# Optimization experiments

Measured on AMD Instinct MI355X. Metric: run time of the kernel, lower is better.

The kernel has to match this reference:

```python
import jax, jax.numpy as jnp
import numpy as np

N = 100000   # nodes
E = 1600000  # edges
IN = 32      # input_dim == num_concepts
H = 128      # h_dim == num_concepts * dim_per_concept
C = 32       # num_concepts
D = 4        # dim_per_concept
G = 32       # g_dim of per-concept MLPs
LAMBDAV = 1e-3


def _spmm(edge_src, edge_dst, edge_val, x):
    # sparse adjacency matmul: out[d] = sum_{edges e: dst(e)=d} val(e) * x[src(e)]
    return jax.ops.segment_sum(edge_val[:, None] * x[edge_src], edge_dst, num_segments=N)


def setup_inputs() -> dict:
    key = jax.random.key(0)
    ks = jax.random.split(key, 20)
    s = lambda shape: 1.0 / np.sqrt(shape[-1] if len(shape) > 1 else 1)
    inp = {
        'X': jax.random.normal(ks[0], (N, IN), jnp.float32),
        'label': jax.random.uniform(ks[1], (N, C), jnp.float32),
        'edge_val': jax.random.uniform(ks[2], (E,), jnp.float32),
        'noise': jax.random.normal(ks[3], (N, C, D), jnp.float32),
        'W_base': jax.random.normal(ks[4], (IN, H), jnp.float32) / np.sqrt(IN),
        'W_mean': jax.random.normal(ks[5], (H, H), jnp.float32) / np.sqrt(H),
        'W_logstd': jax.random.normal(ks[6], (H, H), jnp.float32) / np.sqrt(H),
        'A': 0.05 * jax.random.normal(ks[7], (C, C), jnp.float32),  # keep I - A^T well-conditioned
        'Wz1': jax.random.normal(ks[8], (C, D, G), jnp.float32) / np.sqrt(D),
        'bz1': jax.random.normal(ks[9], (C, G), jnp.float32) * 0.01,
        'Wz2': jax.random.normal(ks[10], (C, G, D), jnp.float32) / np.sqrt(G),
        'bz2': jax.random.normal(ks[11], (C, D), jnp.float32) * 0.01,
        'Wl1': jax.random.normal(ks[12], (C, 1, G), jnp.float32),
        'bl1': jax.random.normal(ks[13], (C, G), jnp.float32) * 0.01,
        'Wl2': jax.random.normal(ks[14], (C, G, 1), jnp.float32) / np.sqrt(G),
        'bl2': jax.random.normal(ks[15], (C, 1), jnp.float32) * 0.01,
        'Wrec': jax.random.normal(ks[16], (H, IN), jnp.float32) / np.sqrt(H),
        'brec': jax.random.normal(ks[17], (IN,), jnp.float32) * 0.01,
        'edge_src': jax.random.randint(ks[18], (E,), 0, N),
        'edge_dst': jax.random.randint(ks[19], (E,), 0, N),
    }
    return inp


def reference(X, label, edge_val, noise, W_base, W_mean, W_logstd, A,
              Wz1, bz1, Wz2, bz2, Wl1, bl1, Wl2, bl2, Wrec, brec,
              edge_src, edge_dst):
    # ---- sparse GCN encoder (x branch): GraphConvSparse = act(spmm(adj, x @ W)) ----
    hidden = jax.nn.relu(_spmm(edge_src, edge_dst, edge_val, X @ W_base))   # [N, H]
    e_m = _spmm(edge_src, edge_dst, edge_val, hidden @ W_mean)              # [N, H]
    _ = _spmm(edge_src, edge_dst, edge_val, hidden @ W_logstd)              # computed then discarded (e_v := ones) in source
    e_m = e_m.reshape(N, C, D)                                              # [N, C, D]

    # ---- CausalDAG: z = (I - A^T)^{-1} epsilon along the concept axis ----
    I = jnp.eye(C, dtype=X.dtype)
    Cmat = jnp.linalg.inv(I - A.T)                                          # [C, C]
    z_m = jnp.einsum('ck,nkd->ncd', Cmat, e_m)                              # [N, C, D]

    # mask: A^T @ x along concept axis
    masked_z_m = jnp.einsum('ck,nkd->ncd', A.T, z_m)                        # [N, C, D]
    masked_label = jnp.einsum('ck,nk->nc', A.T, label)[..., None]           # [N, C, 1]

    # g_z: per-concept MLP Linear(D,G)-ELU-Linear(G,D), weights stacked over concepts
    hz = jax.nn.elu(jnp.einsum('ncd,cdg->ncg', masked_z_m, Wz1) + bz1[None])
    masked_z_m = jnp.einsum('ncg,cgd->ncd', hz, Wz2) + bz2[None]            # [N, C, D]

    # g_label: per-concept MLP Linear(1,G)-ELU-Linear(G,1)
    hl = jax.nn.elu(jnp.einsum('nce,ceg->ncg', masked_label, Wl1) + bl1[None])
    pred_label = (jnp.einsum('ncg,cge->nce', hl, Wl2) + bl2[None])[..., 0]  # [N, C]

    # conditional_sample_gaussian with v = e_v * lambdav, e_v = ones
    z = masked_z_m + jnp.sqrt(jnp.asarray(LAMBDAV, X.dtype)) * noise        # [N, C, D]

    # pred_x / reconst_X head
    rec_x = z.reshape(N, H) @ Wrec + brec                                   # [N, IN]
    return rec_x, pred_label
```

## Files before the change

### kernel.cpp

```cpp
#include <hip/hip_runtime.h>
#include <hip/hip_bf16.h>

#define N_NODES 100000
#define N_EDGES 1600000
#define NBUCK   391

static __device__ __forceinline__ float us2f(unsigned short u) {
    union { unsigned int i; float f; } cv; cv.i = ((unsigned int)u) << 16; return cv.f;
}
static __device__ __forceinline__ unsigned short f2us(float f) {
    __hip_bfloat16 b = __float2bfloat16(f);
    union { __hip_bfloat16 b; unsigned short u; } cv; cv.b = b; return cv.u;
}
static __device__ __forceinline__ float elu_fast(float v) {
    return v > 0.f ? v : (__expf(v) - 1.0f);
}

__global__ __launch_bounds__(64) void k_inv(const float* __restrict__ A,
                                            float* __restrict__ MmT) {
    __shared__ float Af[1024];
    __shared__ float aug[32 * 65];
    __shared__ float fac[32];
    __shared__ float pv_s;
    int t = threadIdx.x;
    for (int i = t; i < 1024; i += 64) Af[i] = A[i];
    __syncthreads();
    for (int i = t; i < 2048; i += 64) {
        int r = i >> 6, c = i & 63;
        float v;
        if (c < 32) v = (r == c ? 1.0f : 0.0f) - Af[c * 32 + r];
        else        v = ((c - 32) == r ? 1.0f : 0.0f);
        aug[r * 65 + c] = v;
    }
    __syncthreads();
    for (int k = 0; k < 32; ++k) {
        if (t == 0) pv_s = 1.0f / aug[k * 65 + k];
        __syncthreads();
        aug[k * 65 + t] *= pv_s;
        __syncthreads();
        if (t < 32) fac[t] = aug[t * 65 + k];
        __syncthreads();
        #pragma unroll 4
        for (int i = t; i < 2048; i += 64) {
            int r = i >> 6, c = i & 63;
            if (r != k) aug[r * 65 + c] -= fac[r] * aug[k * 65 + c];
        }
        __syncthreads();
    }
    for (int i = t; i < 1024; i += 64) {
        int j = i >> 5, c = i & 31;
        float s = 0.f;
        #pragma unroll
        for (int k = 0; k < 32; ++k) s += Af[k * 32 + c] * aug[k * 65 + 32 + j];
        MmT[i] = s;
    }
}

__global__ __launch_bounds__(256) void k_fold(const float* __restrict__ MmT,
                                              const float* __restrict__ Wm,
                                              float* __restrict__ Wcomb) {
    __shared__ float MmTs[1024];
    int tid = threadIdx.x;
    for (int i = tid; i < 1024; i += 256) MmTs[i] = MmT[i];
    __syncthreads();
    int o = blockIdx.x * 256 + tid;
    int h = o >> 5, c = o & 31;
    float4 s = {0.f, 0.f, 0.f, 0.f};
    #pragma unroll
    for (int j = 0; j < 32; ++j) {
        float m = MmTs[j * 32 + c];
        float4 w = ((const float4*)Wm)[h * 32 + j];
        s.x += m * w.x; s.y += m * w.y; s.z += m * w.z; s.w += m * w.w;
    }
    ((float4*)Wcomb)[o] = s;
}

__global__ __launch_bounds__(256) void k_hist(const int* __restrict__ edst,
                                              unsigned int* __restrict__ deg) {
    int e = blockIdx.x * 256 + threadIdx.x;
    atomicAdd(&deg[edst[e]], 1u);
}

__global__ __launch_bounds__(256) void k_scanA(const unsigned int* __restrict__ deg,
                                               unsigned int* __restrict__ row_start,
                                               unsigned int* __restrict__ blk_sums) {
    __shared__ unsigned int sums[256];
    int tid = threadIdx.x;
    int gid = blockIdx.x * 256 + tid;
    uint4 d = ((const uint4*)deg)[gid];
    unsigned int p1 = d.x, p2 = d.x + d.y, p3 = p2 + d.z;
    unsigned int tsum = p3 + d.w;
    sums[tid] = tsum;
    __syncthreads();
    for (int off = 1; off < 256; off <<= 1) {
        unsigned int v = (tid >= off) ? sums[tid - off] : 0u;
        __syncthreads();
        sums[tid] += v;
        __syncthreads();
    }
    unsigned int excl = sums[tid] - tsum;
    int eb = gid * 4;
    if (eb + 0 < N_NODES) row_start[eb + 0] = excl;
    if (eb + 1 < N_NODES) row_start[eb + 1] = excl + p1;
    if (eb + 2 < N_NODES) row_start[eb + 2] = excl + p2;
    if (eb + 3 < N_NODES) row_start[eb + 3] = excl + p3;
    if (tid == 255) blk_sums[blockIdx.x] = sums[255];
}

__global__ __launch_bounds__(128) void k_scanB(unsigned int* __restrict__ blk_sums) {
    __shared__ unsigned int s[128];
    int tid = threadIdx.x;
    unsigned int v = (tid < 98) ? blk_sums[tid] : 0u;
    s[tid] = v;
    __syncthreads();
    for (int off = 1; off < 128; off <<= 1) {
        unsigned int x = (tid >= off) ? s[tid - off] : 0u;
        __syncthreads();
        s[tid] += x;
        __syncthreads();
    }
    if (tid < 98) blk_sums[tid] = s[tid] - v;
}

__global__ __launch_bounds__(256) void k_scanC(unsigned int* __restrict__ row_start,
                                               unsigned int* __restrict__ cursor,
                                               const unsigned int* __restrict__ blk_sums) {
    int tid = threadIdx.x;
    unsigned int off = blk_sums[blockIdx.x];
    int eb = (blockIdx.x * 256 + tid) * 4;
    #pragma unroll
    for (int k = 0; k < 4; ++k) {
        int idx = eb + k;
        if (idx < N_NODES) {
            unsigned int u = row_start[idx] + off;
            row_start[idx] = u;
            cursor[idx] = u;
        }
    }
    if (blockIdx.x == 0 && tid == 0) row_start[N_NODES] = N_EDGES;
}

__global__ __launch_bounds__(256) void k_binit(const unsigned int* __restrict__ row_start,
                                               unsigned int* __restrict__ bucket_cursor) {
    int b = blockIdx.x * 256 + threadIdx.x;
    if (b < NBUCK) bucket_cursor[b] = row_start[b << 8];
}

__global__ __launch_bounds__(256) void k_bucket1(const int* __restrict__ esrc,
                                                 const int* __restrict__ edst,
                                                 const float* __restrict__ evalv,
                                                 unsigned int* __restrict__ bucket_cursor,
                                                 uint2* __restrict__ coarse,
                                                 unsigned char* __restrict__ coarse_dl) {
    __shared__ unsigned int hist[NBUCK];
    __shared__ unsigned int gbase[NBUCK];
    __shared__ unsigned int lcnt[NBUCK];
    int tid = threadIdx.x;
    int e0 = blockIdx.x * 8192;
    for (int i = tid; i < NBUCK; i += 256) { hist[i] = 0u; lcnt[i] = 0u; }
    __syncthreads();
    #pragma unroll 4
    for (int k = 0; k < 32; ++k) {
        int e = e0 + k * 256 + tid;
        if (e < N_EDGES) atomicAdd(&hist[((unsigned)edst[e]) >> 8], 1u);
    }
    __syncthreads();
    for (int b = tid; b < NBUCK; b += 256) {
        unsigned int h = hist[b];
        gbase[b] = h ? atomicAdd(&bucket_cursor[b], h) : 0u;
    }
    __syncthreads();
    #pragma unroll 4
    for (int k = 0; k < 32; ++k) {
        int e = e0 + k * 256 + tid;
        if (e < N_EDGES) {
            unsigned int d = (unsigned)edst[e];
            unsigned int b = d >> 8;
            unsigned int r = atomicAdd(&lcnt[b], 1u);
            unsigned int p = gbase[b] + r;
            uint2 ev;
            ev.x = (unsigned int)esrc[e];
            ev.y = __float_as_uint(evalv[e]);
            coarse[p] = ev;
            coarse_dl[p] = (unsigned char)(d & 255u);
        }
    }
}

__global__ __launch_bounds__(256) void k_bucket2(const unsigned int* __restrict__ row_start,
                                                 const uint2* __restrict__ coarse,
                                                 const unsigned char* __restrict__ coarse_dl,
                                                 unsigned int* __restrict__ cursor,
                                                 uint2* __restrict__ edge_sorted) {
    int b = blockIdx.x;
    unsigned int bs = row_start[b << 8];
    unsigned int be = (b == NBUCK - 1) ? N_EDGES : row_start[(b + 1) << 8];
    unsigned int nbase = (unsigned)b << 8;
    for (unsigned int i = bs + threadIdx.x; i < be; i += 256) {
        uint2 ev = coarse[i];
        unsigned int d = nbase | (unsigned int)coarse_dl[i];
        unsigned int p = atomicAdd(&cursor[d], 1u);
        edge_sorted[p] = ev;
    }
}

__global__ __launch_bounds__(256) void k_fuse1(const unsigned int* __restrict__ row_start,
                                               const uint2* __restrict__ edge_sorted,
                                               const float* __restrict__ X,
                                               const float* __restrict__ Wb,
                                               unsigned short* __restrict__ hidden) {
    __shared__ float Wb_s[4096];
    __shared__ float s1r[8 * 33];
    int tid = threadIdx.x;
    for (int i = tid; i < 1024; i += 256)
        ((float4*)Wb_s)[i] = ((const float4*)Wb)[i];

    int lane = tid & 31;
    int nd = tid >> 5;
    int n = blockIdx.x * 8 + nd;
    unsigned int i = row_start[n], e = row_start[n + 1];
    float a0 = 0.f, a1 = 0.f, a2 = 0.f, a3 = 0.f;
    for (; i + 4 <= e; i += 4) {
        uint2 ea = edge_sorted[i + 0], eb = edge_sorted[i + 1];
        uint2 ec = edge_sorted[i + 2], ed = edge_sorted[i + 3];
        float xa = X[(size_t)ea.x * 32 + lane];
        float xb = X[(size_t)eb.x * 32 + lane];
        float xc = X[(size_t)ec.x * 32 + lane];
        float xd = X[(size_t)ed.x * 32 + lane];
        a0 += __uint_as_float(ea.y) * xa;
        a1 += __uint_as_float(eb.y) * xb;
        a2 += __uint_as_float(ec.y) * xc;
        a3 += __uint_as_float(ed.y) * xd;
    }
    for (; i < e; ++i) {
        uint2 ea = edge_sorted[i];
        a0 += __uint_as_float(ea.y) * X[(size_t)ea.x * 32 + lane];
    }
    s1r[nd * 33 + lane] = (a0 + a1) + (a2 + a3);
    __syncthreads();

    int q = lane * 4;
    float4 acc = {0.f, 0.f, 0.f, 0.f};
    #pragma unroll
    for (int k = 0; k < 32; ++k) {
        float v = s1r[nd * 33 + k];
        float4 w = *(const float4*)&Wb_s[k * 128 + q];
        acc.x += v * w.x; acc.y += v * w.y; acc.z += v * w.z; acc.w += v * w.w;
    }
    ushort4 o;
    o.x = f2us(fmaxf(acc.x, 0.f)); o.y = f2us(fmaxf(acc.y, 0.f));
    o.z = f2us(fmaxf(acc.z, 0.f)); o.w = f2us(fmaxf(acc.w, 0.f));
    *(ushort4*)&hidden[(size_t)n * 128 + q] = o;
}

__global__ __launch_bounds__(256) void k_gather2(const unsigned int* __restrict__ row_start,
                                                 const uint2* __restrict__ edge_sorted,
                                                 const unsigned short* __restrict__ hidden,
                                                 unsigned short* __restrict__ S2) {
    int lane = threadIdx.x & 31;
    int n = blockIdx.x * 8 + (threadIdx.x >> 5);
    unsigned int i = row_start[n], e = row_start[n + 1];
    float4 A0 = {0, 0, 0, 0}, A1 = {0, 0, 0, 0}, A2 = {0, 0, 0, 0}, A3 = {0, 0, 0, 0};
    for (; i + 4 <= e; i += 4) {
        uint2 ea = edge_sorted[i + 0], eb = edge_sorted[i + 1];
        uint2 ec = edge_sorted[i + 2], ed = edge_sorted[i + 3];
        ushort4 ha = *(const ushort4*)&hidden[(size_t)ea.x * 128 + lane * 4];
        ushort4 hb = *(const ushort4*)&hidden[(size_t)eb.x * 128 + lane * 4];
        ushort4 hc = *(const ushort4*)&hidden[(size_t)ec.x * 128 + lane * 4];
        ushort4 hd = *(const ushort4*)&hidden[(size_t)ed.x * 128 + lane * 4];
        float va = __uint_as_float(ea.y), vb = __uint_as_float(eb.y);
        float vc = __uint_as_float(ec.y), vd = __uint_as_float(ed.y);
        A0.x += va * us2f(ha.x); A0.y += va * us2f(ha.y); A0.z += va * us2f(ha.z); A0.w += va * us2f(ha.w);
        A1.x += vb * us2f(hb.x); A1.y += vb * us2f(hb.y); A1.z += vb * us2f(hb.z); A1.w += vb * us2f(hb.w);
        A2.x += vc * us2f(hc.x); A2.y += vc * us2f(hc.y); A2.z += vc * us2f(hc.z); A2.w += vc * us2f(hc.w);
        A3.x += vd * us2f(hd.x); A3.y += vd * us2f(hd.y); A3.z += vd * us2f(hd.z); A3.w += vd * us2f(hd.w);
    }
    for (; i < e; ++i) {
        uint2 ea = edge_sorted[i];
        float v = __uint_as_float(ea.y);
        ushort4 h = *(const ushort4*)&hidden[(size_t)ea.x * 128 + lane * 4];
        A0.x += v * us2f(h.x); A0.y += v * us2f(h.y); A0.z += v * us2f(h.z); A0.w += v * us2f(h.w);
    }
    float4 acc;
    acc.x = (A0.x + A1.x) + (A2.x + A3.x);
    acc.y = (A0.y + A1.y) + (A2.y + A3.y);
    acc.z = (A0.z + A1.z) + (A2.z + A3.z);
    acc.w = (A0.w + A1.w) + (A2.w + A3.w);
    ushort4 o;
    o.x = f2us(acc.x); o.y = f2us(acc.y); o.z = f2us(acc.z); o.w = f2us(acc.w);
    *(ushort4*)&S2[(size_t)n * 128 + lane * 4] = o;
}

__global__ __launch_bounds__(256) void k_gemm2(const unsigned short* __restrict__ S2,
                                               const float* __restrict__ Wc,
                                               unsigned short* __restrict__ mt4) {
    __shared__ float Wc_s[128 * 64];
    __shared__ float S2s[32 * 132];
    __shared__ unsigned short Tt[64 * 40];
    int tid = threadIdx.x;
    int rb = blockIdx.x >> 1;
    int j0 = (blockIdx.x & 1) * 64;
    int n0 = rb * 32;
    for (int idx = tid; idx < 2048; idx += 256) {
        int k = idx >> 4, jq = idx & 15;
        *(float4*)&Wc_s[k * 64 + jq * 4] = *(const float4*)&Wc[k * 128 + j0 + jq * 4];
    }
    for (int idx = tid; idx < 1024; idx += 256) {
        int r = idx >> 5, kq = idx & 31;
        ushort4 h = *(const ushort4*)&S2[(size_t)(n0 + r) * 128 + kq * 4];
        float4 f = {us2f(h.x), us2f(h.y), us2f(h.z), us2f(h.w)};
        *(float4*)&S2s[r * 132 + kq * 4] = f;
    }
    __syncthreads();
    int q = (tid & 15) * 4;
    int r0 = tid >> 4;
    float4 a0 = {0, 0, 0, 0}, a1 = {0, 0, 0, 0};
    for (int k4 = 0; k4 < 128; k4 += 4) {
        float4 s0 = *(const float4*)&S2s[r0 * 132 + k4];
        float4 s1 = *(const float4*)&S2s[(r0 + 16) * 132 + k4];
        #pragma unroll
        for (int kk = 0; kk < 4; ++kk) {
            float v0 = (&s0.x)[kk];
            float v1 = (&s1.x)[kk];
            float4 w = *(const float4*)&Wc_s[(k4 + kk) * 64 + q];
            a0.x += v0 * w.x; a0.y += v0 * w.y; a0.z += v0 * w.z; a0.w += v0 * w.w;
            a1.x += v1 * w.x; a1.y += v1 * w.y; a1.z += v1 * w.z; a1.w += v1 * w.w;
        }
    }
    #pragma unroll
    for (int c = 0; c < 4; ++c) {
        Tt[(q + c) * 40 + r0]      = f2us((&a0.x)[c]);
        Tt[(q + c) * 40 + r0 + 16] = f2us((&a1.x)[c]);
    }
    __syncthreads();
    int cc = tid >> 4;
    int r  = (tid & 15) * 2;
    int cg = (j0 >> 2) + cc;
    #pragma unroll
    for (int rr = 0; rr < 2; ++rr) {
        ushort4 o;
        o.x = Tt[(cc * 4 + 0) * 40 + r + rr];
        o.y = Tt[(cc * 4 + 1) * 40 + r + rr];
        o.z = Tt[(cc * 4 + 2) * 40 + r + rr];
        o.w = Tt[(cc * 4 + 3) * 40 + r + rr];
        *(ushort4*)&mt4[((size_t)cg * N_NODES + n0 + r + rr) * 4] = o;
    }
}

__global__ __launch_bounds__(256) void k_noisew(const float* __restrict__ noise,
                                                const float* __restrict__ Wrec,
                                                const float* __restrict__ brec,
                                                float* __restrict__ noiseW) {
    __shared__ float Wr[4096];
    __shared__ float Ns[64 * 132];
    __shared__ float brs[32];
    int tid = threadIdx.x;
    int n0 = blockIdx.x * 64;
    const float SQ = 0.03162277660168379f;
    for (int i = tid; i < 1024; i += 256)
        ((float4*)Wr)[i] = ((const float4*)Wrec)[i];
    if (tid < 32) brs[tid] = brec[tid];
    for (int i = tid; i < 1024; i += 256) {
        int row = i >> 4, u8 = i & 15;
        int n = n0 + row;
        float4 f0, f1;
        if (n < N_NODES) {
            f0 = ((const float4*)(noise + (size_t)n * 128))[u8 * 2];
            f1 = ((const float4*)(noise + (size_t)n * 128))[u8 * 2 + 1];
        } else {
            f0 = make_float4(0.f, 0.f, 0.f, 0.f);
            f1 = f0;
        }
        *(float4*)&Ns[row * 132 + u8 * 8]     = make_float4(SQ * f0.x, SQ * f0.y, SQ * f0.z, SQ * f0.w);
        *(float4*)&Ns[row * 132 + u8 * 8 + 4] = make_float4(SQ * f1.x, SQ * f1.y, SQ * f1.z, SQ * f1.w);
    }
    __syncthreads();
    int r = tid >> 2, q = (tid & 3) * 8;
    float4 acc0 = {0, 0, 0, 0}, acc1 = {0, 0, 0, 0};
    for (int k = 0; k < 128; ++k) {
        float nv = Ns[r * 132 + k];
        float4 w0 = *(const float4*)&Wr[k * 32 + q];
        float4 w1 = *(const float4*)&Wr[k * 32 + q + 4];
        acc0.x += nv * w0.x; acc0.y += nv * w0.y; acc0.z += nv * w0.z; acc0.w += nv * w0.w;
        acc1.x += nv * w1.x; acc1.y += nv * w1.y; acc1.z += nv * w1.z; acc1.w += nv * w1.w;
    }
    int n = n0 + r;
    if (n < N_NODES) {
        acc0.x += brs[q];     acc0.y += brs[q + 1]; acc0.z += brs[q + 2]; acc0.w += brs[q + 3];
        acc1.x += brs[q + 4]; acc1.y += brs[q + 5]; acc1.z += brs[q + 6]; acc1.w += brs[q + 7];
        ((float4*)(noiseW + (size_t)n * 32 + q))[0] = acc0;
        ((float4*)(noiseW + (size_t)n * 32 + q + 4))[0] = acc1;
    }
}

__global__ __launch_bounds__(512) void k_nodez(const unsigned short* __restrict__ mt4,
                                               const float* __restrict__ Wz1,
                                               const float* __restrict__ bz1,
                                               const float* __restrict__ Wz2,
                                               const float* __restrict__ bz2,
                                               const float* __restrict__ Wrec,
                                               const float* __restrict__ noiseW,
                                               float* __restrict__ out) {
    __shared__ float scr[3 * 128 * 34];
    int tid = threadIdx.x;
    int lt  = tid & 127;
    int qq  = tid >> 7;
    int c0  = __builtin_amdgcn_readfirstlane(qq * 8);
    int n = blockIdx.x * 128 + lt;
    bool ok = n < N_NODES;
    int m = ok ? n : (N_NODES - 1);

    const float4* W1 = (const float4*)Wz1;
    const float4* B1 = (const float4*)bz1;
    const float4* W2 = (const float4*)Wz2;
    const float4* B2 = (const float4*)bz2;
    const float4* WR = (const float4*)Wrec;

    float4 o0 = {0,0,0,0}, o1 = {0,0,0,0}, o2 = {0,0,0,0}, o3 = {0,0,0,0};
    float4 o4v = {0,0,0,0}, o5 = {0,0,0,0}, o6 = {0,0,0,0}, o7 = {0,0,0,0};

    ushort4 mz = *(const ushort4*)&mt4[((size_t)c0 * N_NODES + m) * 4];

    for (int cc = 0; cc < 8; ++cc) {
        int c = c0 + cc;
        int cn = (cc < 7) ? (c + 1) : c;
        ushort4 nmz = *(const ushort4*)&mt4[((size_t)cn * N_NODES + m) * 4];
        float a0 = us2f(mz.x), a1 = us2f(mz.y), a2 = us2f(mz.z), a3 = us2f(mz.w);

        float4 zb = B2[c];
        float4 z = zb;
        #pragma unroll
        for (int g4 = 0; g4 < 8; ++g4) {
            float4 w0 = W1[c * 32 + g4];
            float4 w1 = W1[c * 32 + 8 + g4];
            float4 w2 = W1[c * 32 + 16 + g4];
            float4 w3 = W1[c * 32 + 24 + g4];
            float4 bb = B1[c * 8 + g4];
            float4 v;
            v.x = bb.x + a0 * w0.x + a1 * w1.x + a2 * w2.x + a3 * w3.x;
            v.y = bb.y + a0 * w0.y + a1 * w1.y + a2 * w2.y + a3 * w3.y;
            v.z = bb.z + a0 * w0.z + a1 * w1.z + a2 * w2.z + a3 * w3.z;
            v.w = bb.w + a0 * w0.w + a1 * w1.w + a2 * w2.w + a3 * w3.w;
            v.x = elu_fast(v.x); v.y = elu_fast(v.y); v.z = elu_fast(v.z); v.w = elu_fast(v.w);
            float4 u0 = W2[c * 32 + g4 * 4 + 0];
            float4 u1 = W2[c * 32 + g4 * 4 + 1];
            float4 u2 = W2[c * 32 + g4 * 4 + 2];
            float4 u3 = W2[c * 32 + g4 * 4 + 3];
            z.x += v.x * u0.x + v.y * u1.x + v.z * u2.x + v.w * u3.x;
            z.y += v.x * u0.y + v.y * u1.y + v.z * u2.y + v.w * u3.y;
            z.z += v.x * u0.z + v.y * u1.z + v.z * u2.z + v.w * u3.z;
            z.w += v.x * u0.w + v.y * u1.w + v.z * u2.w + v.w * u3.w;
        }
        #pragma unroll
        for (int d = 0; d < 4; ++d) {
            float zv = (&z.x)[d];
            const float4* wr = &WR[(c * 4 + d) * 8];
            float4 r0 = wr[0], r1 = wr[1], r2 = wr[2], r3 = wr[3];
            float4 r4 = wr[4], r5 = wr[5], r6 = wr[6], r7 = wr[7];
            o0.x += zv * r0.x; o0.y += zv * r0.y; o0.z += zv * r0.z; o0.w += zv * r0.w;
            o1.x += zv * r1.x; o1.y += zv * r1.y; o1.z += zv * r1.z; o1.w += zv * r1.w;
            o2.x += zv * r2.x; o2.y += zv * r2.y; o2.z += zv * r2.z; o2.w += zv * r2.w;
            o3.x += zv * r3.x; o3.y += zv * r3.y; o3.z += zv * r3.z; o3.w += zv * r3.w;
            o4v.x += zv * r4.x; o4v.y += zv * r4.y; o4v.z += zv * r4.z; o4v.w += zv * r4.w;
            o5.x += zv * r5.x; o5.y += zv * r5.y; o5.z += zv * r5.z; o5.w += zv * r5.w;
            o6.x += zv * r6.x; o6.y += zv * r6.y; o6.z += zv * r6.z; o6.w += zv * r6.w;
            o7.x += zv * r7.x; o7.y += zv * r7.y; o7.z += zv * r7.z; o7.w += zv * r7.w;
        }
        mz = nmz;
    }

    __syncthreads();
    if (qq != 0) {
        float* p = &scr[((qq - 1) * 128 + lt) * 34];
        *(float2*)&p[0]  = make_float2(o0.x, o0.y);  *(float2*)&p[2]  = make_float2(o0.z, o0.w);
        *(float2*)&p[4]  = make_float2(o1.x, o1.y);  *(float2*)&p[6]  = make_float2(o1.z, o1.w);
        *(float2*)&p[8]  = make_float2(o2.x, o2.y);  *(float2*)&p[10] = make_float2(o2.z, o2.w);
        *(float2*)&p[12] = make_float2(o3.x, o3.y);  *(float2*)&p[14] = make_float2(o3.z, o3.w);
        *(float2*)&p[16] = make_float2(o4v.x, o4v.y); *(float2*)&p[18] = make_float2(o4v.z, o4v.w);
        *(float2*)&p[20] = make_float2(o5.x, o5.y);  *(float2*)&p[22] = make_float2(o5.z, o5.w);
        *(float2*)&p[24] = make_float2(o6.x, o6.y);  *(float2*)&p[26] = make_float2(o6.z, o6.w);
        *(float2*)&p[28] = make_float2(o7.x, o7.y);  *(float2*)&p[30] = make_float2(o7.z, o7.w);
    }
    __syncthreads();
    if (qq == 0 && ok) {
        const float* pA = &scr[lt * 34];
        const float* pB = &scr[(128 + lt) * 34];
        const float* pC = &scr[(256 + lt) * 34];
        const float4* nw = (const float4*)(noiseW + (size_t)n * 32);
        float4* po = (float4*)(out + (size_t)n * 32);
        float4 w, t;
        w = nw[0];
        t.x = o0.x + pA[0] + pB[0] + pC[0] + w.x;   t.y = o0.y + pA[1] + pB[1] + pC[1] + w.y;
        t.z = o0.z + pA[2] + pB[2] + pC[2] + w.z;   t.w = o0.w + pA[3] + pB[3] + pC[3] + w.w;
        po[0] = t;
        w = nw[1];
        t.x = o1.x + pA[4] + pB[4] + pC[4] + w.x;   t.y = o1.y + pA[5] + pB[5] + pC[5] + w.y;
        t.z = o1.z + pA[6] + pB[6] + pC[6] + w.z;   t.w = o1.w + pA[7] + pB[7] + pC[7] + w.w;
        po[1] = t;
        w = nw[2];
        t.x = o2.x + pA[8] + pB[8] + pC[8] + w.x;   t.y = o2.y + pA[9] + pB[9] + pC[9] + w.y;
        t.z = o2.z + pA[10] + pB[10] + pC[10] + w.z; t.w = o2.w + pA[11] + pB[11] + pC[11] + w.w;
        po[2] = t;
        w = nw[3];
        t.x = o3.x + pA[12] + pB[12] + pC[12] + w.x; t.y = o3.y + pA[13] + pB[13] + pC[13] + w.y;
        t.z = o3.z + pA[14] + pB[14] + pC[14] + w.z; t.w = o3.w + pA[15] + pB[15] + pC[15] + w.w;
        po[3] = t;
        w = nw[4];
        t.x = o4v.x + pA[16] + pB[16] + pC[16] + w.x; t.y = o4v.y + pA[17] + pB[17] + pC[17] + w.y;
        t.z = o4v.z + pA[18] + pB[18] + pC[18] + w.z; t.w = o4v.w + pA[19] + pB[19] + pC[19] + w.w;
        po[4] = t;
        w = nw[5];
        t.x = o5.x + pA[20] + pB[20] + pC[20] + w.x; t.y = o5.y + pA[21] + pB[21] + pC[21] + w.y;
        t.z = o5.z + pA[22] + pB[22] + pC[22] + w.z; t.w = o5.w + pA[23] + pB[23] + pC[23] + w.w;
        po[5] = t;
        w = nw[6];
        t.x = o6.x + pA[24] + pB[24] + pC[24] + w.x; t.y = o6.y + pA[25] + pB[25] + pC[25] + w.y;
        t.z = o6.z + pA[26] + pB[26] + pC[26] + w.z; t.w = o6.w + pA[27] + pB[27] + pC[27] + w.w;
        po[6] = t;
        w = nw[7];
        t.x = o7.x + pA[28] + pB[28] + pC[28] + w.x; t.y = o7.y + pA[29] + pB[29] + pC[29] + w.y;
        t.z = o7.z + pA[30] + pB[30] + pC[30] + w.z; t.w = o7.w + pA[31] + pB[31] + pC[31] + w.w;
        po[7] = t;
    }
}

__global__ __launch_bounds__(256) void k_label(const float* __restrict__ label,
                                               const float* __restrict__ A,
                                               const float* __restrict__ Wl1,
                                               const float* __restrict__ bl1,
                                               const float* __restrict__ Wl2,
                                               const float* __restrict__ bl2,
                                               float* __restrict__ out) {
    __shared__ float As[1024], Wl1s[1024], bl1s[1024], Wl2s[1024], bl2s[32];
    int tid = threadIdx.x;
    for (int i = tid; i < 1024; i += 256) {
        As[i] = A[i];
        Wl1s[i] = Wl1[i];
        bl1s[i] = bl1[i];
        Wl2s[i] = Wl2[i];
    }
    if (tid < 32) bl2s[tid] = bl2[tid];
    __syncthreads();

    int n = blockIdx.x * 256 + tid;
    bool ok = n < N_NODES;
    int nn = ok ? n : (N_NODES - 1);

    float lab[32];
    #pragma unroll
    for (int q = 0; q < 8; ++q) {
        float4 lv = ((const float4*)(label + (size_t)nn * 32))[q];
        lab[q * 4 + 0] = lv.x; lab[q * 4 + 1] = lv.y;
        lab[q * 4 + 2] = lv.z; lab[q * 4 + 3] = lv.w;
    }
    float pred[32];
    for (int c = 0; c < 32; ++c) {
        float ml = 0.f;
        #pragma unroll
        for (int k = 0; k < 32; ++k) ml += As[k * 32 + c] * lab[k];
        float p = bl2s[c];
        #pragma unroll
        for (int g = 0; g < 32; ++g) {
            float h = elu_fast(ml * Wl1s[c * 32 + g] + bl1s[c * 32 + g]);
            p += h * Wl2s[c * 32 + g];
        }
        pred[c] = p;
    }
    if (ok) {
        #pragma unroll
        for (int q = 0; q < 8; ++q) {
            float4 v = {pred[q * 4 + 0], pred[q * 4 + 1], pred[q * 4 + 2], pred[q * 4 + 3]};
            ((float4*)(out + (size_t)N_NODES * 32 + (size_t)n * 32))[q] = v;
        }
    }
}

extern "C" void kernel_launch(void* const* d_in, const int* in_sizes, int n_in,
                              void* d_out, int out_size, void* d_ws, size_t ws_size,
                              hipStream_t stream) {
    const float* X      = (const float*)d_in[0];
    const float* label  = (const float*)d_in[1];
    const float* evalv  = (const float*)d_in[2];
    const float* noise  = (const float*)d_in[3];
    const float* W_base = (const float*)d_in[4];
    const float* W_mean = (const float*)d_in[5];
    const float* A      = (const float*)d_in[7];
    const float* Wz1    = (const float*)d_in[8];
    const float* bz1    = (const float*)d_in[9];
    const float* Wz2    = (const float*)d_in[10];
    const float* bz2    = (const float*)d_in[11];
    const float* Wl1    = (const float*)d_in[12];
    const float* bl1    = (const float*)d_in[13];
    const float* Wl2    = (const float*)d_in[14];
    const float* bl2    = (const float*)d_in[15];
    const float* Wrec   = (const float*)d_in[16];
    const float* brec   = (const float*)d_in[17];
    const int* esrc = (const int*)d_in[18];
    const int* edst = (const int*)d_in[19];
    float* out = (float*)d_out;

    char* ws = (char*)d_ws;
    float*          Wcomb       = (float*)(ws);
    float*          MmT         = (float*)(ws + 65536);
    unsigned int*   blk_sums    = (unsigned int*)(ws + 69632);
    unsigned int*   deg         = (unsigned int*)(ws + 70656);
    unsigned int*   bucket_cursor = (unsigned int*)(ws + 70656);
    unsigned int*   row_start   = (unsigned int*)(ws + 472064);
    unsigned int*   cursor      = (unsigned int*)(ws + 873984);
    uint2*          edge_sorted = (uint2*)(ws + 1273984);
    uint2*          coarse      = (uint2*)(ws + 14073984);
    unsigned char*  coarse_dl   = (unsigned char*)(ws + 26873984);
    unsigned short* hidden      = (unsigned short*)(ws + 14073984);
    unsigned short* mt4         = (unsigned short*)(ws + 14073984);
    unsigned short* S2          = (unsigned short*)(ws + 39673984);
    float*          noiseW      = (float*)(ws + 39673984);

    hipMemsetAsync(deg, 0, 100352 * sizeof(unsigned int), stream);
    k_inv<<<1, 64, 0, stream>>>(A, MmT);
    k_fold<<<16, 256, 0, stream>>>(MmT, W_mean, Wcomb);
    k_hist<<<N_EDGES / 256, 256, 0, stream>>>(edst, deg);
    k_scanA<<<98, 256, 0, stream>>>(deg, row_start, blk_sums);
    k_scanB<<<1, 128, 0, stream>>>(blk_sums);
    k_scanC<<<98, 256, 0, stream>>>(row_start, cursor, blk_sums);
    k_binit<<<2, 256, 0, stream>>>(row_start, bucket_cursor);
    k_bucket1<<<(N_EDGES + 8191) / 8192, 256, 0, stream>>>(esrc, edst, evalv,
                                                           bucket_cursor, coarse, coarse_dl);
    k_bucket2<<<NBUCK, 256, 0, stream>>>(row_start, coarse, coarse_dl, cursor, edge_sorted);
    k_fuse1<<<N_NODES / 8, 256, 0, stream>>>(row_start, edge_sorted, X, W_base, hidden);
    k_gather2<<<N_NODES / 8, 256, 0, stream>>>(row_start, edge_sorted, hidden, S2);
    k_gemm2<<<(N_NODES / 32) * 2, 256, 0, stream>>>(S2, Wcomb, mt4);
    k_noisew<<<(N_NODES + 63) / 64, 256, 0, stream>>>(noise, Wrec, brec, noiseW);
    k_nodez<<<(N_NODES + 127) / 128, 512, 0, stream>>>(mt4,
                                                       Wz1, bz1, Wz2, bz2,
                                                       Wrec, noiseW, out);
    k_label<<<(N_NODES + 255) / 256, 256, 0, stream>>>(label, A, Wl1, bl1, Wl2, bl2, out);
}
```

Measured before the change: 748.9 us.

## Replace per-node degree histogram and global scan with bucket-level histogram and in-block scan

Replaces the global per-node degree histogram (1.6M global atomics) and the three-kernel prefix scan with a bucket-level histogram that uses shared-memory atomics and a single-block scan over 391 buckets. Each bucket2 block now builds a local per-node histogram and scan in shared memory to produce row_start and scatter edges with LDS atomics instead of global cursor atomics. This cuts kernel launches and global atomic traffic in the CSR build, at the cost of an extra pass over coarse_dl in bucket2.

```diff
diff --git a/kernel.cpp b/kernel.cpp
--- a/kernel.cpp
+++ b/kernel.cpp
@@ -4,6 +4,7 @@
 #define N_NODES 100000
 #define N_EDGES 1600000
 #define NBUCK   391
+#define EHIST_G 196
 
 static __device__ __forceinline__ float us2f(unsigned short u) {
     union { unsigned int i; float f; } cv; cv.i = ((unsigned int)u) << 16; return cv.f;
@@ -75,75 +76,45 @@
     ((float4*)Wcomb)[o] = s;
 }
 
-__global__ __launch_bounds__(256) void k_hist(const int* __restrict__ edst,
-                                              unsigned int* __restrict__ deg) {
-    int e = blockIdx.x * 256 + threadIdx.x;
-    atomicAdd(&deg[edst[e]], 1u);
-}
-
-__global__ __launch_bounds__(256) void k_scanA(const unsigned int* __restrict__ deg,
-                                               unsigned int* __restrict__ row_start,
-                                               unsigned int* __restrict__ blk_sums) {
-    __shared__ unsigned int sums[256];
-    int tid = threadIdx.x;
-    int gid = blockIdx.x * 256 + tid;
-    uint4 d = ((const uint4*)deg)[gid];
-    unsigned int p1 = d.x, p2 = d.x + d.y, p3 = p2 + d.z;
-    unsigned int tsum = p3 + d.w;
-    sums[tid] = tsum;
-    __syncthreads();
-    for (int off = 1; off < 256; off <<= 1) {
-        unsigned int v = (tid >= off) ? sums[tid - off] : 0u;
-        __syncthreads();
-        sums[tid] += v;
-        __syncthreads();
-    }
-    unsigned int excl = sums[tid] - tsum;
-    int eb = gid * 4;
-    if (eb + 0 < N_NODES) row_start[eb + 0] = excl;
-    if (eb + 1 < N_NODES) row_start[eb + 1] = excl + p1;
-    if (eb + 2 < N_NODES) row_start[eb + 2] = excl + p2;
-    if (eb + 3 < N_NODES) row_start[eb + 3] = excl + p3;
-    if (tid == 255) blk_sums[blockIdx.x] = sums[255];
-}
-
-__global__ __launch_bounds__(128) void k_scanB(unsigned int* __restrict__ blk_sums) {
-    __shared__ unsigned int s[128];
-    int tid = threadIdx.x;
-    unsigned int v = (tid < 98) ? blk_sums[tid] : 0u;
+__global__ __launch_bounds__(256) void k_bhist(const int* __restrict__ edst,
+                                               unsigned int* __restrict__ bucket_deg) {
+    __shared__ unsigned int h[NBUCK];
+    int tid = threadIdx.x;
+    int e0 = blockIdx.x * 8192;
+    for (int i = tid; i < NBUCK; i += 256) h[i] = 0u;
+    __syncthreads();
+    #pragma unroll 4
+    for (int k = 0; k < 32; ++k) {
+        int e = e0 + k * 256 + tid;
+        if (e < N_EDGES) atomicAdd(&h[((unsigned)edst[e]) >> 8], 1u);
+    }
+    __syncthreads();
+    for (int b = tid; b < NBUCK; b += 256) {
+        unsigned int v = h[b];
+        if (v) atomicAdd(&bucket_deg[b], v);
+    }
+}
+
+__global__ __launch_bounds__(512) void k_bscan(const unsigned int* __restrict__ bucket_deg,
+                                               unsigned int* __restrict__ bucket_start,
+                                               unsigned int* __restrict__ bucket_cursor) {
+    __shared__ unsigned int s[512];
+    int tid = threadIdx.x;
+    unsigned int v = (tid < NBUCK) ? bucket_deg[tid] : 0u;
     s[tid] = v;
     __syncthreads();
-    for (int off = 1; off < 128; off <<= 1) {
+    for (int off = 1; off < 512; off <<= 1) {
         unsigned int x = (tid >= off) ? s[tid - off] : 0u;
         __syncthreads();
         s[tid] += x;
         __syncthreads();
     }
-    if (tid < 98) blk_sums[tid] = s[tid] - v;
-}
-
-__global__ __launch_bounds__(256) void k_scanC(unsigned int* __restrict__ row_start,
-                                               unsigned int* __restrict__ cursor,
-                                               const unsigned int* __restrict__ blk_sums) {
-    int tid = threadIdx.x;
-    unsigned int off = blk_sums[blockIdx.x];
-    int eb = (blockIdx.x * 256 + tid) * 4;
-    #pragma unroll
-    for (int k = 0; k < 4; ++k) {
-        int idx = eb + k;
-        if (idx < N_NODES) {
-            unsigned int u = row_start[idx] + off;
-            row_start[idx] = u;
-            cursor[idx] = u;
-        }
-    }
-    if (blockIdx.x == 0 && tid == 0) row_start[N_NODES] = N_EDGES;
-}
-
-__global__ __launch_bounds__(256) void k_binit(const unsigned int* __restrict__ row_start,
-                                               unsigned int* __restrict__ bucket_cursor) {
-    int b = blockIdx.x * 256 + threadIdx.x;
-    if (b < NBUCK) bucket_cursor[b] = row_start[b << 8];
+    if (tid < NBUCK) {
+        unsigned int excl = s[tid] - v;
+        bucket_start[tid] = excl;
+        bucket_cursor[tid] = excl;
+    }
+    if (tid == 0) bucket_start[NBUCK] = N_EDGES;
 }
 
 __global__ __launch_bounds__(256) void k_bucket1(const int* __restrict__ esrc,
@@ -187,20 +158,42 @@
     }
 }
 
-__global__ __launch_bounds__(256) void k_bucket2(const unsigned int* __restrict__ row_start,
+__global__ __launch_bounds__(256) void k_bucket2(const unsigned int* __restrict__ bucket_start,
                                                  const uint2* __restrict__ coarse,
                                                  const unsigned char* __restrict__ coarse_dl,
-                                                 unsigned int* __restrict__ cursor,
+                                                 unsigned int* __restrict__ row_start,
                                                  uint2* __restrict__ edge_sorted) {
+    __shared__ unsigned int h[256];
+    __shared__ unsigned int sc[256];
     int b = blockIdx.x;
-    unsigned int bs = row_start[b << 8];
-    unsigned int be = (b == NBUCK - 1) ? N_EDGES : row_start[(b + 1) << 8];
-    unsigned int nbase = (unsigned)b << 8;
-    for (unsigned int i = bs + threadIdx.x; i < be; i += 256) {
+    int tid = threadIdx.x;
+    unsigned int bs = bucket_start[b];
+    unsigned int be = bucket_start[b + 1];
+    h[tid] = 0u;
+    __syncthreads();
+    for (unsigned int i = bs + tid; i < be; i += 256)
+        atomicAdd(&h[coarse_dl[i]], 1u);
+    __syncthreads();
+    unsigned int v = h[tid];
+    sc[tid] = v;
+    __syncthreads();
+    for (int off = 1; off < 256; off <<= 1) {
+        unsigned int x = (tid >= off) ? sc[tid - off] : 0u;
+        __syncthreads();
+        sc[tid] += x;
+        __syncthreads();
+    }
+    unsigned int excl = sc[tid] - v;
+    int node = (b << 8) + tid;
+    if (node < N_NODES) row_start[node] = bs + excl;
+    if (b == 0 && tid == 0) row_start[N_NODES] = N_EDGES;
+    h[tid] = excl;
+    __syncthreads();
+    for (unsigned int i = bs + tid; i < be; i += 256) {
         uint2 ev = coarse[i];
-        unsigned int d = nbase | (unsigned int)coarse_dl[i];
-        unsigned int p = atomicAdd(&cursor[d], 1u);
-        edge_sorted[p] = ev;
+        unsigned int dl = coarse_dl[i];
+        unsigned int r = atomicAdd(&h[dl], 1u);
+        edge_sorted[bs + r] = ev;
     }
 }
 
@@ -600,32 +593,29 @@
     float* out = (float*)d_out;
 
     char* ws = (char*)d_ws;
-    float*          Wcomb       = (float*)(ws);
-    float*          MmT         = (float*)(ws + 65536);
-    unsigned int*   blk_sums    = (unsigned int*)(ws + 69632);
-    unsigned int*   deg         = (unsigned int*)(ws + 70656);
-    unsigned int*   bucket_cursor = (unsigned int*)(ws + 70656);
-    unsigned int*   row_start   = (unsigned int*)(ws + 472064);
-    unsigned int*   cursor      = (unsigned int*)(ws + 873984);
-    uint2*          edge_sorted = (uint2*)(ws + 1273984);
-    uint2*          coarse      = (uint2*)(ws + 14073984);
-    unsigned char*  coarse_dl   = (unsigned char*)(ws + 26873984);
-    unsigned short* hidden      = (unsigned short*)(ws + 14073984);
-    unsigned short* mt4         = (unsigned short*)(ws + 14073984);
-    unsigned short* S2          = (unsigned short*)(ws + 39673984);
-    float*          noiseW      = (float*)(ws + 39673984);
-
-    hipMemsetAsync(deg, 0, 100352 * sizeof(unsigned int), stream);
+    float*          Wcomb        = (float*)(ws);
+    float*          MmT          = (float*)(ws + 65536);
+    unsigned int*   bucket_deg   = (unsigned int*)(ws + 69632);
+    unsigned int*   bucket_start = (unsigned int*)(ws + 71680);
+    unsigned int*   bucket_cursor= (unsigned int*)(ws + 73728);
+    unsigned int*   row_start    = (unsigned int*)(ws + 472064);
+    uint2*          edge_sorted  = (uint2*)(ws + 1273984);
+    uint2*          coarse       = (uint2*)(ws + 14073984);
+    unsigned char*  coarse_dl    = (unsigned char*)(ws + 26873984);
+    unsigned short* hidden       = (unsigned short*)(ws + 14073984);
+    unsigned short* mt4          = (unsigned short*)(ws + 14073984);
+    unsigned short* S2           = (unsigned short*)(ws + 39673984);
+    float*          noiseW       = (float*)(ws + 39673984);
+
+    hipMemsetAsync(bucket_deg, 0, 2048, stream);
     k_inv<<<1, 64, 0, stream>>>(A, MmT);
     k_fold<<<16, 256, 0, stream>>>(MmT, W_mean, Wcomb);
-    k_hist<<<N_EDGES / 256, 256, 0, stream>>>(edst, deg);
-    k_scanA<<<98, 256, 0, stream>>>(deg, row_start, blk_sums);
-    k_scanB<<<1, 128, 0, stream>>>(blk_sums);
-    k_scanC<<<98, 256, 0, stream>>>(row_start, cursor, blk_sums);
-    k_binit<<<2, 256, 0, stream>>>(row_start, bucket_cursor);
-    k_bucket1<<<(N_EDGES + 8191) / 8192, 256, 0, stream>>>(esrc, edst, evalv,
-                                                           bucket_cursor, coarse, coarse_dl);
-    k_bucket2<<<NBUCK, 256, 0, stream>>>(row_start, coarse, coarse_dl, cursor, edge_sorted);
+    k_bhist<<<EHIST_G, 256, 0, stream>>>(edst, bucket_deg);
+    k_bscan<<<1, 512, 0, stream>>>(bucket_deg, bucket_start, bucket_cursor);
+    k_bucket1<<<EHIST_G, 256, 0, stream>>>(esrc, edst, evalv,
+                                           bucket_cursor, coarse, coarse_dl);
+    k_bucket2<<<NBUCK, 256, 0, stream>>>(bucket_start, coarse, coarse_dl,
+                                         row_start, edge_sorted);
     k_fuse1<<<N_NODES / 8, 256, 0, stream>>>(row_start, edge_sorted, X, W_base, hidden);
     k_gather2<<<N_NODES / 8, 256, 0, stream>>>(row_start, edge_sorted, hidden, S2);
     k_gemm2<<<(N_NODES / 32) * 2, 256, 0, stream>>>(S2, Wcomb, mt4);
```

Measured after the change: 679.3 us. 9.3% less time.
